# Performance work log

Measured on AMD Instinct MI355X. Metric: run time of the kernel, lower is better.

## Reference

```python
import jax, jax.numpy as jnp
import numpy as np

V0 = 25; WIN = 3; NS = 6; EPS = 1e-5

def _build_scales():
    # ring graph on 25 joints (matches A_binary in init_kwargs)
    A = np.zeros((V0, V0), np.float32)
    for i in range(V0):
        A[i, (i + 1) % V0] = 1.0; A[(i + 1) % V0, i] = 1.0
    AL = np.tile(A + np.eye(V0, dtype=A.dtype), (WIN, WIN))  # spatial-temporal graph (75x75)
    I = np.eye(len(AL), dtype=AL.dtype)
    def shell(k):
        return np.minimum(np.linalg.matrix_power(AL + I, k), 1) - np.minimum(np.linalg.matrix_power(AL + I, k - 1), 1)
    def kadj(k):
        return I.copy() if k == 0 else shell(k) + I  # with_self=True
    def norm(g):
        dinv = np.power(g.sum(-1), -0.5)
        Dm = np.eye(len(g)) * dinv
        return (Dm @ g @ Dm).astype(np.float32)
    def klap(k):
        if k == 0:
            return I.astype(np.float32)
        Ak = shell(k)
        D = Ak.sum(-1)
        Dm = np.eye(len(D)) * np.power(D, -0.5)
        return (Dm @ (np.eye(len(D)) * (D + 2) - Ak) @ Dm).astype(np.float32)
    A_scales = np.concatenate([norm(kadj(k)) for k in range(NS)])  # (NS*75, 75)
    B_scales = np.concatenate([klap(k) for k in range(NS)])        # (NS*75, 75)
    return jnp.asarray(A_scales), jnp.asarray(B_scales)

def _bn(x, g, b):
    # BatchNorm2d in training mode: batch stats over (N, T, V)
    m = x.mean(axis=(0, 2, 3), keepdims=True)
    v = x.var(axis=(0, 2, 3), keepdims=True)
    return (x - m) * jax.lax.rsqrt(v + EPS) * g[None, :, None, None] + b[None, :, None, None]

def setup_inputs():
    key = jax.random.key(0)
    ks = jax.random.split(key, 4)
    N, C, T = 8, 96, 128
    A_scales, B_scales = _build_scales()
    d_in = C * NS * 2
    return {
        'x': jax.random.normal(ks[0], (N, C, T, V0), jnp.float32),
        'A_scales': A_scales,
        'B_scales': B_scales,
        'A_res': jax.random.uniform(ks[1], A_scales.shape, jnp.float32, -1e-6, 1e-6),
        'W_mlp': jax.random.normal(ks[2], (C, d_in), jnp.float32) / np.sqrt(d_in),
        'b_mlp': jnp.zeros((C,), jnp.float32),
        'g1': jnp.ones((C,), jnp.float32),
        'bt1': jnp.zeros((C,), jnp.float32),
        'W_out': jax.random.normal(ks[3], (C, C, WIN), jnp.float32) / np.sqrt(C * WIN),
        'b_out': jnp.zeros((C,), jnp.float32),
        'g2': jnp.ones((C,), jnp.float32),
        'bt2': jnp.zeros((C,), jnp.float32),
    }

def _forward(x, A_scales, B_scales, A_res, W_mlp, b_mlp, g1, bt1, W_out, b_out, g2, bt2):
    N, C, T, V = x.shape
    xp = jnp.pad(x, ((0, 0), (0, 0), (1, 1), (0, 0)))
    xu = jnp.stack([xp[:, :, w:w + T, :] for w in range(WIN)], axis=3).reshape(N, C, T, WIN * V)
    VL = WIN * V
    A = A_scales + A_res
    B = B_scales + A_res
    def agg(M):
        a = jnp.einsum('vu,nctu->nctv', M, xu)               # (N, C, T, NS*VL)
        a = a.reshape(N, C, T, NS, VL).transpose(0, 3, 1, 2, 4)
        return a.reshape(N, NS * C, T, VL)
    h = jnp.concatenate([agg(A), agg(B)], axis=1)            # (N, 2*NS*C, T, VL)
    # MLP: 1x1 conv -> ReLU -> BN
    h = jnp.einsum('oi,nitv->notv', W_mlp, h) + b_mlp[None, :, None, None]
    h = _bn(jax.nn.relu(h), g1, bt1)
    h = jax.nn.relu(h)                                       # gcn: act(mlp + residual(=0))
    h = h.reshape(N, C, T, WIN, V)
    out = jnp.einsum('oiw,nitwv->notv', W_out, h) + b_out[None, :, None, None]
    return _bn(out, g2, bt2)

def reference(x, A_scales, B_scales, A_res, W_mlp, b_mlp, g1, bt1, W_out, b_out, g2, bt2):
    return _forward(x, A_scales, B_scales, A_res, W_mlp, b_mlp, g1, bt1, W_out, b_out, g2, bt2)
```

## Files before the change

### kernel.cpp

```cpp
#include <hip/hip_runtime.h>


#define NB 8
#define CB 96
#define TB 128
#define VB 25
#define VLB 75
#define EPSB 1e-5f
#define XRS 104
#define TMS 104
#define HBS 296

typedef __attribute__((ext_vector_type(8))) short bf16x8;
typedef __attribute__((ext_vector_type(4))) float f32x4;

__device__ inline unsigned short f2bf(float f) {
  unsigned int u = __float_as_uint(f);
  u = (u + 0x7FFFu + ((u >> 16) & 1u)) >> 16;
  return (unsigned short)u;
}
__device__ inline float bf2f(unsigned short u) {
  return __uint_as_float(((unsigned int)u) << 16);
}

__global__ __launch_bounds__(256) void k0_init(
    const float* __restrict__ As, const float* __restrict__ Bs,
    const float* __restrict__ Ar, const float* __restrict__ Wm,
    const float* __restrict__ Wo,
    unsigned short* __restrict__ ABsw, unsigned short* __restrict__ Wsw,
    unsigned short* __restrict__ Wosw, float* __restrict__ stats) {
  int i = blockIdx.x * 256 + threadIdx.x;
  if (i < 110592) {
    int ps = i / 9216, r = i % 9216;
    int wv = r / 1536, r2 = r % 1536;
    int kk = r2 / 512, r3 = r2 % 512;
    int lane = r3 / 8, j = r3 % 8;
    int o = wv * 16 + (lane & 15);
    int c = kk * 32 + (lane >> 4) * 8 + j;
    Wsw[i] = f2bf(Wm[o * 1152 + ps * 96 + c]);
  }
  if (i < 92160) {
    int ps = i / 7680, r = i % 7680;
    int nt = r / 1536, r2 = r % 1536;
    int kk = r2 / 512, r3 = r2 % 512;
    int lane = r3 / 8, j = r3 % 8;
    int u = nt * 16 + (lane & 15);
    int up = kk * 32 + (lane >> 4) * 8 + j;
    float v = 0.f;
    if (u < 75 && up < 75) {
      int path = ps / 6, s = ps % 6;
      int idx = (s * 75 + u) * 75 + up;
      v = (path == 0 ? As[idx] : Bs[idx]) + Ar[idx];
    }
    ABsw[i] = f2bf(v);
  }
  if (i < 27648) {
    int wv = i / 4608, r = i % 4608;
    int kk = r / 512, r3 = r % 512;
    int lane = r3 / 8, j = r3 % 8;
    int o = wv * 16 + (lane & 15);
    int k = kk * 32 + (lane >> 4) * 8 + j;
    Wosw[i] = f2bf(Wo[o * 288 + k]);
  }
  if (i < 384) stats[i] = 0.f;
}

__global__ __launch_bounds__(384, 2) void k1t2(
    const float* __restrict__ x, const unsigned short* __restrict__ ABsw,
    const unsigned short* __restrict__ Wsw, const float* __restrict__ bm,
    unsigned short* __restrict__ h_relu, float* __restrict__ stats1) {
  __shared__ unsigned short xraw[112 * XRS];
  __shared__ unsigned short tmp_s[2][96 * TMS];
  __shared__ float st1s[96], st2s[96];
  const int tid = threadIdx.x;
  const int n = blockIdx.x >> 6, t0 = (blockIdx.x & 63) * 2;
  const int wave = tid >> 6, lane = tid & 63;
  const int l15 = lane & 15, quad = lane >> 4, q8 = quad * 8;
  const int wrow16 = wave * 16;

  for (int idx = tid; idx < 96 * 112; idx += 384) {
    int c = idx / 112, r = idx - c * 112;
    float v = 0.f;
    if (r < 100) {
      int tt = t0 - 1 + r / 25, vv = r % 25;
      if (tt >= 0 && tt < TB) v = x[((n * CB + c) * TB + tt) * VB + vv];
    }
    xraw[r * XRS + c] = f2bf(v);
  }
  for (int idx = tid; idx < 2 * 96 * 16; idx += 384) {
    int b = idx / (96 * 16), rem = idx - b * 96 * 16;
    tmp_s[b][(rem / 16) * TMS + 80 + rem % 16] = 0;
  }
  __syncthreads();

  const f32x4 zf = {0.f, 0.f, 0.f, 0.f};
  f32x4 acc2[2][5];
#pragma unroll
  for (int d = 0; d < 2; ++d)
#pragma unroll
    for (int nt = 0; nt < 5; ++nt) acc2[d][nt] = zf;

  const unsigned short* Wbase = Wsw + wave * 1536 + lane * 8;
  const unsigned short* Bbase = ABsw + lane * 8;

#pragma unroll
  for (int ps = 0; ps < 12; ++ps) {
    bf16x8 wa[3];
#pragma unroll
    for (int kk = 0; kk < 3; ++kk)
      wa[kk] = *reinterpret_cast<const bf16x8*>(Wbase + ps * 9216 + kk * 512);
    bf16x8 bf[15];
#pragma unroll
    for (int i = 0; i < 15; ++i)
      bf[i] = *reinterpret_cast<const bf16x8*>(Bbase + ps * 7680 + i * 512);

    f32x4 acc1[5];
#pragma unroll
    for (int nt = 0; nt < 5; ++nt) acc1[nt] = zf;
#pragma unroll
    for (int kk = 0; kk < 3; ++kk)
#pragma unroll
      for (int nt = 0; nt < 5; ++nt) {
        bf16x8 b = *reinterpret_cast<const bf16x8*>(&xraw[(nt * 16 + l15) * XRS + kk * 32 + q8]);
        acc1[nt] = __builtin_amdgcn_mfma_f32_16x16x32_bf16(wa[kk], b, acc1[nt], 0, 0, 0);
      }
#pragma unroll
    for (int nt = 0; nt < 5; ++nt) {
      int col = nt * 16 + l15;
#pragma unroll
      for (int r = 0; r < 4; ++r) {
        unsigned short v = (col < 75) ? f2bf(acc1[nt][r]) : (unsigned short)0;
        tmp_s[0][(wrow16 + quad * 4 + r) * TMS + col] = v;
      }
    }
#pragma unroll
    for (int nt = 0; nt < 5; ++nt) acc1[nt] = zf;
#pragma unroll
    for (int kk = 0; kk < 3; ++kk)
#pragma unroll
      for (int nt = 0; nt < 5; ++nt) {
        bf16x8 b = *reinterpret_cast<const bf16x8*>(&xraw[(25 + nt * 16 + l15) * XRS + kk * 32 + q8]);
        acc1[nt] = __builtin_amdgcn_mfma_f32_16x16x32_bf16(wa[kk], b, acc1[nt], 0, 0, 0);
      }
#pragma unroll
    for (int nt = 0; nt < 5; ++nt) {
      int col = nt * 16 + l15;
#pragma unroll
      for (int r = 0; r < 4; ++r) {
        unsigned short v = (col < 75) ? f2bf(acc1[nt][r]) : (unsigned short)0;
        tmp_s[1][(wrow16 + quad * 4 + r) * TMS + col] = v;
      }
    }

#pragma unroll
    for (int kk = 0; kk < 3; ++kk) {
      bf16x8 a0 = *reinterpret_cast<const bf16x8*>(&tmp_s[0][(wrow16 + l15) * TMS + kk * 32 + q8]);
#pragma unroll
      for (int nt = 0; nt < 5; ++nt)
        acc2[0][nt] = __builtin_amdgcn_mfma_f32_16x16x32_bf16(a0, bf[nt * 3 + kk], acc2[0][nt], 0, 0, 0);
      bf16x8 a1 = *reinterpret_cast<const bf16x8*>(&tmp_s[1][(wrow16 + l15) * TMS + kk * 32 + q8]);
#pragma unroll
      for (int nt = 0; nt < 5; ++nt)
        acc2[1][nt] = __builtin_amdgcn_mfma_f32_16x16x32_bf16(a1, bf[nt * 3 + kk], acc2[1][nt], 0, 0, 0);
    }
  }

  const int orow = wrow16 + quad * 4;
  float s1[4] = {0.f, 0.f, 0.f, 0.f}, s2[4] = {0.f, 0.f, 0.f, 0.f};
#pragma unroll
  for (int d = 0; d < 2; ++d) {
    const int t = t0 + d;
#pragma unroll
    for (int r = 0; r < 4; ++r) {
      const int o = orow + r;
      const float bias = bm[o];
      unsigned short* hp = h_relu + ((n * TB + t) * CB + o) * VLB;
#pragma unroll
      for (int nt = 0; nt < 5; ++nt) {
        int u = nt * 16 + l15;
        if (u < VLB) {
          float v = acc2[d][nt][r] + bias;
          v = v > 0.f ? v : 0.f;
          hp[u] = f2bf(v);
          s1[r] += v;
          s2[r] += v * v;
        }
      }
    }
  }
#pragma unroll
  for (int off = 1; off < 16; off <<= 1) {
#pragma unroll
    for (int r = 0; r < 4; ++r) {
      s1[r] += __shfl_xor(s1[r], off, 64);
      s2[r] += __shfl_xor(s2[r], off, 64);
    }
  }
  if (l15 == 0) {
#pragma unroll
    for (int r = 0; r < 4; ++r) { st1s[orow + r] = s1[r]; st2s[orow + r] = s2[r]; }
  }
  __syncthreads();
  if (tid < 96) {
    atomicAdd(&stats1[tid], st1s[tid]);
    atomicAdd(&stats1[96 + tid], st2s[tid]);
  }
}

__global__ __launch_bounds__(384) void k3n(
    const unsigned short* __restrict__ h_relu, const float* __restrict__ stats1,
    const float* __restrict__ g1, const float* __restrict__ bt1,
    const unsigned short* __restrict__ Wosw, const float* __restrict__ bo,
    float* __restrict__ out_pre) {
  __shared__ unsigned short hnb[2][32 * HBS];
  __shared__ float a1s[96], b1s[96];
  const int tid = threadIdx.x;
  const int n = blockIdx.x >> 6, t0 = (blockIdx.x & 63) * 2;

  if (tid < 96) {
    const float inv = 1.f / (8.f * 128.f * 75.f);
    float m = stats1[tid] * inv;
    float var = stats1[96 + tid] * inv - m * m;
    float a = g1[tid] * rsqrtf(var + EPSB);
    a1s[tid] = a;
    b1s[tid] = bt1[tid] - m * a;
  }
  for (int idx = tid; idx < 2 * 7 * HBS; idx += 384) {
    int d = idx / (7 * HBS), rm = idx % (7 * HBS);
    hnb[d][25 * HBS + rm] = 0;
  }
  __syncthreads();

  const unsigned short* hp = h_relu + (n * TB + t0) * (CB * VLB);
  for (int i8 = tid; i8 < 1800; i8 += 384) {
    bf16x8 v = *reinterpret_cast<const bf16x8*>(hp + i8 * 8);
    int ee = i8 * 8;
    int d = (ee >= 7200) ? 1 : 0;
    int rem = ee - d * 7200;
#pragma unroll
    for (int j = 0; j < 8; ++j) {
      int e = rem + j;
      int i = e / 75, u = e - i * 75;
      float val = a1s[i] * bf2f((unsigned short)v[j]) + b1s[i];
      val = val > 0.f ? val : 0.f;
      int w = u / 25, vv = u - w * 25;
      hnb[d][vv * HBS + i * 3 + w] = f2bf(val);
    }
  }
  __syncthreads();

  const int wave = tid >> 6, lane = tid & 63;
  const int l15 = lane & 15, quad = lane >> 4, q8 = quad * 8;
  const f32x4 zf = {0.f, 0.f, 0.f, 0.f};
  f32x4 acc[2][2] = {{zf, zf}, {zf, zf}};
  const unsigned short* Apw = Wosw + wave * 4608 + lane * 8;
#pragma unroll
  for (int kk = 0; kk < 9; ++kk) {
    bf16x8 a = *reinterpret_cast<const bf16x8*>(Apw + kk * 512);
#pragma unroll
    for (int d = 0; d < 2; ++d) {
      bf16x8 b0 = *reinterpret_cast<const bf16x8*>(&hnb[d][l15 * HBS + kk * 32 + q8]);
      bf16x8 b1 = *reinterpret_cast<const bf16x8*>(&hnb[d][(16 + l15) * HBS + kk * 32 + q8]);
      acc[d][0] = __builtin_amdgcn_mfma_f32_16x16x32_bf16(a, b0, acc[d][0], 0, 0, 0);
      acc[d][1] = __builtin_amdgcn_mfma_f32_16x16x32_bf16(a, b1, acc[d][1], 0, 0, 0);
    }
  }

  const int orow = wave * 16 + quad * 4;
#pragma unroll
  for (int d = 0; d < 2; ++d) {
#pragma unroll
    for (int nt = 0; nt < 2; ++nt) {
      int v = nt * 16 + l15;
      if (v < VB) {
#pragma unroll
        for (int r = 0; r < 4; ++r) {
          const int o = orow + r;
          out_pre[((n * CB + o) * TB + t0 + d) * VB + v] = acc[d][nt][r] + bo[o];
        }
      }
    }
  }
}

__global__ __launch_bounds__(256) void k4_stats(
    const float* __restrict__ out_pre, float* __restrict__ stats2) {
  __shared__ float ws1[4], ws2[4];
  const int tid = threadIdx.x;
  const int o = blockIdx.x % CB, p = blockIdx.x / CB;
  float s1 = 0.f, s2 = 0.f;
#pragma unroll
  for (int k = 0; k < 2; ++k) {
    const int n = 2 * p + k;
    const f32x4* base = reinterpret_cast<const f32x4*>(out_pre + (n * CB + o) * (TB * VB));
    for (int idx = tid; idx < TB * VB / 4; idx += 256) {
      f32x4 v = base[idx];
#pragma unroll
      for (int j = 0; j < 4; ++j) { s1 += v[j]; s2 += v[j] * v[j]; }
    }
  }
#pragma unroll
  for (int off = 1; off < 64; off <<= 1) {
    s1 += __shfl_xor(s1, off, 64);
    s2 += __shfl_xor(s2, off, 64);
  }
  const int wave = tid >> 6;
  if ((tid & 63) == 0) { ws1[wave] = s1; ws2[wave] = s2; }
  __syncthreads();
  if (tid == 0) {
    float r1 = ws1[0] + ws1[1] + ws1[2] + ws1[3];
    float r2 = ws2[0] + ws2[1] + ws2[2] + ws2[3];
    atomicAdd(&stats2[o], r1);
    atomicAdd(&stats2[96 + o], r2);
  }
}

__global__ __launch_bounds__(256) void k5_bn2(
    const float* __restrict__ out_pre, const float* __restrict__ stats2,
    const float* __restrict__ g2, const float* __restrict__ bt2,
    float* __restrict__ out) {
  int idx = blockIdx.x * 256 + threadIdx.x;
  if (idx >= NB * CB * TB * VB / 4) return;
  int o = (idx / (TB * VB / 4)) % CB;
  const float inv = 1.f / (8.f * 128.f * 25.f);
  float m = stats2[o] * inv;
  float var = stats2[96 + o] * inv - m * m;
  float a = g2[o] * rsqrtf(var + EPSB);
  float b = bt2[o] - m * a;
  f32x4 vin = reinterpret_cast<const f32x4*>(out_pre)[idx];
  f32x4 vo;
#pragma unroll
  for (int j = 0; j < 4; ++j) vo[j] = a * vin[j] + b;
  reinterpret_cast<f32x4*>(out)[idx] = vo;
}

extern "C" void kernel_launch(void* const* d_in, const int* in_sizes, int n_in,
                              void* d_out, int out_size, void* d_ws, size_t ws_size,
                              hipStream_t stream) {
  const float* x   = (const float*)d_in[0];
  const float* As  = (const float*)d_in[1];
  const float* Bs  = (const float*)d_in[2];
  const float* Ar  = (const float*)d_in[3];
  const float* Wm  = (const float*)d_in[4];
  const float* bm  = (const float*)d_in[5];
  const float* g1  = (const float*)d_in[6];
  const float* bt1 = (const float*)d_in[7];
  const float* Wo  = (const float*)d_in[8];
  const float* bo  = (const float*)d_in[9];
  const float* g2  = (const float*)d_in[10];
  const float* bt2 = (const float*)d_in[11];
  float* out = (float*)d_out;

  char* base = (char*)d_ws;
  unsigned short* HR   = (unsigned short*)base;
  float* out_pre       = (float*)(base + 14745600);
  unsigned short* ABsw = (unsigned short*)(base + 24576000);
  unsigned short* Wsw  = (unsigned short*)(base + 24760320);
  unsigned short* Wosw = (unsigned short*)(base + 24981504);
  float* stats         = (float*)(base + 25036800);
  float* stats1 = stats, *stats2 = stats + 192;

  k0_init<<<432, 256, 0, stream>>>(As, Bs, Ar, Wm, Wo, ABsw, Wsw, Wosw, stats);
  k1t2<<<NB * TB / 2, 384, 0, stream>>>(x, ABsw, Wsw, bm, HR, stats1);
  k3n<<<NB * TB / 2, 384, 0, stream>>>(HR, stats1, g1, bt1, Wosw, bo, out_pre);
  k4_stats<<<CB * 4, 256, 0, stream>>>(out_pre, stats2);
  k5_bn2<<<(NB * CB * TB * VB / 4 + 255) / 256, 256, 0, stream>>>(out_pre, stats2, g2, bt2, out);
}
```

Measured before the change: 182.7 us.

## Transpose first-stage MFMA to per-wave scratch and store h_relu in consumer layout

The first GEMM now swaps its operands so each lane holds four consecutive columns. Results are packed into 64-bit bf16 stores in a per-wave private LDS scratch instead of scattered 16-bit stores into a shared tile. The intermediate h_relu is written directly in the (v, channel*3+window) layout the second kernel needs. That kernel can then do plain vectorized 128-bit LDS stores instead of a scattered transpose. This trades more scattered global stores in the first kernel for cheaper LDS traffic in both kernels, and adds sched barriers that constrain instruction scheduling.

```diff
diff --git a/kernel.cpp b/kernel.cpp
--- a/kernel.cpp
+++ b/kernel.cpp
@@ -8,11 +8,14 @@
 #define VLB 75
 #define EPSB 1e-5f
 #define XRS 104
-#define TMS 104
+#define T2S 104
 #define HBS 296
 
 typedef __attribute__((ext_vector_type(8))) short bf16x8;
+typedef __attribute__((ext_vector_type(4))) short short4v;
 typedef __attribute__((ext_vector_type(4))) float f32x4;
+typedef __attribute__((ext_vector_type(2))) unsigned int uint2v;
+typedef __attribute__((ext_vector_type(4))) unsigned int uint4v;
 
 __device__ inline unsigned short f2bf(float f) {
   unsigned int u = __float_as_uint(f);
@@ -21,6 +24,9 @@
 }
 __device__ inline float bf2f(unsigned short u) {
   return __uint_as_float(((unsigned int)u) << 16);
+}
+__device__ inline unsigned pack2bf(float lo, float hi) {
+  return (unsigned)f2bf(lo) | ((unsigned)f2bf(hi) << 16);
 }
 
 __global__ __launch_bounds__(256) void k0_init(
@@ -70,7 +76,7 @@
     const unsigned short* __restrict__ Wsw, const float* __restrict__ bm,
     unsigned short* __restrict__ h_relu, float* __restrict__ stats1) {
   __shared__ unsigned short xraw[112 * XRS];
-  __shared__ unsigned short tmp_s[2][96 * TMS];
+  __shared__ unsigned short tmp2[6][2][16 * T2S];
   __shared__ float st1s[96], st2s[96];
   const int tid = threadIdx.x;
   const int n = blockIdx.x >> 6, t0 = (blockIdx.x & 63) * 2;
@@ -87,9 +93,10 @@
     }
     xraw[r * XRS + c] = f2bf(v);
   }
-  for (int idx = tid; idx < 2 * 96 * 16; idx += 384) {
-    int b = idx / (96 * 16), rem = idx - b * 96 * 16;
-    tmp_s[b][(rem / 16) * TMS + 80 + rem % 16] = 0;
+  for (int idx = tid; idx < 6 * 2 * 256; idx += 384) {
+    int w = idx >> 9, rm = idx & 511;
+    int d = rm >> 8, e = rm & 255;
+    tmp2[w][d][(e >> 4) * T2S + 80 + (e & 15)] = 0;
   }
   __syncthreads();
 
@@ -102,6 +109,10 @@
 
   const unsigned short* Wbase = Wsw + wave * 1536 + lane * 8;
   const unsigned short* Bbase = ABsw + lane * 8;
+  unsigned short* tw0 = &tmp2[wave][0][l15 * T2S + quad * 4];
+  unsigned short* tw1 = &tmp2[wave][1][l15 * T2S + quad * 4];
+  const unsigned short* tr0 = &tmp2[wave][0][l15 * T2S + q8];
+  const unsigned short* tr1 = &tmp2[wave][1][l15 * T2S + q8];
 
 #pragma unroll
   for (int ps = 0; ps < 12; ++ps) {
@@ -121,67 +132,69 @@
     for (int kk = 0; kk < 3; ++kk)
 #pragma unroll
       for (int nt = 0; nt < 5; ++nt) {
-        bf16x8 b = *reinterpret_cast<const bf16x8*>(&xraw[(nt * 16 + l15) * XRS + kk * 32 + q8]);
-        acc1[nt] = __builtin_amdgcn_mfma_f32_16x16x32_bf16(wa[kk], b, acc1[nt], 0, 0, 0);
+        bf16x8 a = *reinterpret_cast<const bf16x8*>(&xraw[(nt * 16 + l15) * XRS + kk * 32 + q8]);
+        acc1[nt] = __builtin_amdgcn_mfma_f32_16x16x32_bf16(a, wa[kk], acc1[nt], 0, 0, 0);
       }
 #pragma unroll
     for (int nt = 0; nt < 5; ++nt) {
-      int col = nt * 16 + l15;
-#pragma unroll
-      for (int r = 0; r < 4; ++r) {
-        unsigned short v = (col < 75) ? f2bf(acc1[nt][r]) : (unsigned short)0;
-        tmp_s[0][(wrow16 + quad * 4 + r) * TMS + col] = v;
+      unsigned p01 = pack2bf(acc1[nt][0], acc1[nt][1]);
+      unsigned p23 = pack2bf(acc1[nt][2], acc1[nt][3]);
+      *reinterpret_cast<short4v*>(tw0 + nt * 16) =
+          __builtin_bit_cast(short4v, (uint2v){p01, p23});
+    }
+#pragma unroll
+    for (int nt = 0; nt < 5; ++nt) acc1[nt] = zf;
+#pragma unroll
+    for (int kk = 0; kk < 3; ++kk)
+#pragma unroll
+      for (int nt = 0; nt < 5; ++nt) {
+        bf16x8 a = *reinterpret_cast<const bf16x8*>(&xraw[(25 + nt * 16 + l15) * XRS + kk * 32 + q8]);
+        acc1[nt] = __builtin_amdgcn_mfma_f32_16x16x32_bf16(a, wa[kk], acc1[nt], 0, 0, 0);
       }
-    }
-#pragma unroll
-    for (int nt = 0; nt < 5; ++nt) acc1[nt] = zf;
-#pragma unroll
-    for (int kk = 0; kk < 3; ++kk)
-#pragma unroll
-      for (int nt = 0; nt < 5; ++nt) {
-        bf16x8 b = *reinterpret_cast<const bf16x8*>(&xraw[(25 + nt * 16 + l15) * XRS + kk * 32 + q8]);
-        acc1[nt] = __builtin_amdgcn_mfma_f32_16x16x32_bf16(wa[kk], b, acc1[nt], 0, 0, 0);
-      }
 #pragma unroll
     for (int nt = 0; nt < 5; ++nt) {
-      int col = nt * 16 + l15;
-#pragma unroll
-      for (int r = 0; r < 4; ++r) {
-        unsigned short v = (col < 75) ? f2bf(acc1[nt][r]) : (unsigned short)0;
-        tmp_s[1][(wrow16 + quad * 4 + r) * TMS + col] = v;
-      }
-    }
+      unsigned p01 = pack2bf(acc1[nt][0], acc1[nt][1]);
+      unsigned p23 = pack2bf(acc1[nt][2], acc1[nt][3]);
+      *reinterpret_cast<short4v*>(tw1 + nt * 16) =
+          __builtin_bit_cast(short4v, (uint2v){p01, p23});
+    }
+
+    asm volatile("" ::: "memory");
+    __builtin_amdgcn_sched_barrier(0);
 
 #pragma unroll
     for (int kk = 0; kk < 3; ++kk) {
-      bf16x8 a0 = *reinterpret_cast<const bf16x8*>(&tmp_s[0][(wrow16 + l15) * TMS + kk * 32 + q8]);
+      bf16x8 a0 = *reinterpret_cast<const bf16x8*>(tr0 + kk * 32);
 #pragma unroll
       for (int nt = 0; nt < 5; ++nt)
         acc2[0][nt] = __builtin_amdgcn_mfma_f32_16x16x32_bf16(a0, bf[nt * 3 + kk], acc2[0][nt], 0, 0, 0);
-      bf16x8 a1 = *reinterpret_cast<const bf16x8*>(&tmp_s[1][(wrow16 + l15) * TMS + kk * 32 + q8]);
+      bf16x8 a1 = *reinterpret_cast<const bf16x8*>(tr1 + kk * 32);
 #pragma unroll
       for (int nt = 0; nt < 5; ++nt)
         acc2[1][nt] = __builtin_amdgcn_mfma_f32_16x16x32_bf16(a1, bf[nt * 3 + kk], acc2[1][nt], 0, 0, 0);
     }
+
+    asm volatile("" ::: "memory");
+    __builtin_amdgcn_sched_barrier(0);
   }
 
   const int orow = wrow16 + quad * 4;
   float s1[4] = {0.f, 0.f, 0.f, 0.f}, s2[4] = {0.f, 0.f, 0.f, 0.f};
+  unsigned short* hp = h_relu + (unsigned)(n * TB + t0) * 7200;
 #pragma unroll
   for (int d = 0; d < 2; ++d) {
-    const int t = t0 + d;
 #pragma unroll
     for (int r = 0; r < 4; ++r) {
       const int o = orow + r;
       const float bias = bm[o];
-      unsigned short* hp = h_relu + ((n * TB + t) * CB + o) * VLB;
 #pragma unroll
       for (int nt = 0; nt < 5; ++nt) {
         int u = nt * 16 + l15;
         if (u < VLB) {
           float v = acc2[d][nt][r] + bias;
           v = v > 0.f ? v : 0.f;
-          hp[u] = f2bf(v);
+          int w = u / 25, vv = u - w * 25;
+          hp[d * 7200 + vv * 288 + o * 3 + w] = f2bf(v);
           s1[r] += v;
           s2[r] += v * v;
         }
@@ -231,21 +244,25 @@
   }
   __syncthreads();
 
-  const unsigned short* hp = h_relu + (n * TB + t0) * (CB * VLB);
+  const unsigned short* hp = h_relu + (unsigned)(n * TB + t0) * 7200;
   for (int i8 = tid; i8 < 1800; i8 += 384) {
     bf16x8 v = *reinterpret_cast<const bf16x8*>(hp + i8 * 8);
-    int ee = i8 * 8;
-    int d = (ee >= 7200) ? 1 : 0;
-    int rem = ee - d * 7200;
+    int e = i8 * 8;
+    int d = e / 7200;
+    int er = e - d * 7200;
+    int vv = er / 288, c = er - vv * 288;
+    float f[8];
 #pragma unroll
     for (int j = 0; j < 8; ++j) {
-      int e = rem + j;
-      int i = e / 75, u = e - i * 75;
-      float val = a1s[i] * bf2f((unsigned short)v[j]) + b1s[i];
-      val = val > 0.f ? val : 0.f;
-      int w = u / 25, vv = u - w * 25;
-      hnb[d][vv * HBS + i * 3 + w] = f2bf(val);
-    }
+      int ic = (c + j) / 3;
+      float val = a1s[ic] * bf2f((unsigned short)v[j]) + b1s[ic];
+      f[j] = val > 0.f ? val : 0.f;
+    }
+    unsigned dw0 = pack2bf(f[0], f[1]);
+    unsigned dw1 = pack2bf(f[2], f[3]);
+    unsigned dw2 = pack2bf(f[4], f[5]);
+    unsigned dw3 = pack2bf(f[6], f[7]);
+    *reinterpret_cast<uint4v*>(&hnb[d][vv * HBS + c]) = (uint4v){dw0, dw1, dw2, dw3};
   }
   __syncthreads();
 
```

After: 180.3 us. No clear change (-1.3%).
